# Kernel optimization log

Hardware: AMD Instinct MI355X
Metric: run time of the kernel (lower is better)

The kernel has to match this reference:

```python
import jax, jax.numpy as jnp
import numpy as np

LN_EPS = 1e-12
CHEB_K = 3
HIDDEN = 64


def _layernorm(x, w, b):
    m = jnp.mean(x, axis=-1, keepdims=True)
    v = jnp.mean((x - m) ** 2, axis=-1, keepdims=True)
    return (x - m) / jnp.sqrt(v + LN_EPS) * w + b


def _magcn(x, node_emb, time_emb, ln_w, ln_b, W_pool, b_pool):
    # x: [B,N,C]; node_emb: [N,D]; W_pool: [D,K,C,O]; b_pool: [D,O]
    e = _layernorm(node_emb + time_emb[None, :], ln_w, ln_b)  # dropout = identity (eval)
    supports = jax.nn.softmax(e @ e.T, axis=1)                # [N,N]
    N = e.shape[0]
    Ts = [jnp.eye(N, dtype=x.dtype), supports]
    for _ in range(2, CHEB_K):
        Ts.append(2.0 * supports @ Ts[-1] - Ts[-2])
    S = jnp.stack(Ts, axis=0)                                 # [K,N,N]
    weights = jnp.einsum('nd,dkio->nkio', e, W_pool)          # [N,K,C,O]
    bias = e @ b_pool                                         # [N,O]
    x_g = jnp.einsum('knm,bmc->bnkc', S, x)                   # [B,N,K,C]
    return jnp.einsum('bnki,nkio->bno', x_g, weights) + bias  # [B,N,O]


def setup_inputs() -> dict:
    key = jax.random.key(0)
    ks = jax.random.split(key, 10)
    B, N, C, H, D = 64, 1024, 64, HIDDEN, 16
    return {
        'x': jax.random.normal(ks[0], (B, N, C), jnp.float32),
        'norm_dis_matrix': jax.random.uniform(ks[1], (N, N), jnp.float32),
        'state': jax.random.normal(ks[2], (B, N, H), jnp.float32),
        'node_embeddings': jax.random.normal(ks[3], (N, D), jnp.float32),
        'node_flows': jax.random.normal(ks[4], (B, N), jnp.float32),
        'time_embeddings': jax.random.normal(ks[5], (D,), jnp.float32),
        'gate_W': jax.random.normal(ks[6], (D, CHEB_K, C + H, 2 * H), jnp.float32) * 0.1,
        'gate_b': jax.random.normal(ks[7], (D, 2 * H), jnp.float32) * 0.1,
        'gate_ln_w': jnp.ones((D,), jnp.float32),
        'gate_ln_b': jnp.zeros((D,), jnp.float32),
        'update_W': jax.random.normal(ks[8], (D, CHEB_K, C + H, H), jnp.float32) * 0.1,
        'update_b': jax.random.normal(ks[9], (D, H), jnp.float32) * 0.1,
        'update_ln_w': jnp.ones((D,), jnp.float32),
        'update_ln_b': jnp.zeros((D,), jnp.float32),
    }


def reference(x, norm_dis_matrix, state, node_embeddings, node_flows, time_embeddings,
              gate_W, gate_b, gate_ln_w, gate_ln_b,
              update_W, update_b, update_ln_w, update_ln_b):
    inp_state = jnp.concatenate([x, state], axis=-1)  # [B,N,C+H]
    z_r = jax.nn.sigmoid(_magcn(inp_state, node_embeddings, time_embeddings,
                                gate_ln_w, gate_ln_b, gate_W, gate_b))
    z, r = z_r[..., :HIDDEN], z_r[..., HIDDEN:]
    candidate = jnp.concatenate([x, z * state], axis=-1)
    hc = jnp.tanh(_magcn(candidate, node_embeddings, time_embeddings,
                         update_ln_w, update_ln_b, update_W, update_b))
    return r * state + (1.0 - r) * hc
```

## Files before the change

### kernel.cpp

```cpp
#include <hip/hip_runtime.h>
#include <hip/hip_bf16.h>

typedef __hip_bfloat16 bf16;
typedef __attribute__((ext_vector_type(8))) short bf16x8;
typedef __attribute__((ext_vector_type(4))) float f32x4;

constexpr int Bn = 64;
constexpr int Nn = 1024;
constexpr int Dd = 16;
constexpr int Cc = 64;
constexpr int Hh = 64;
constexpr int CI = 128;
constexpr int OG = 128;
constexpr int OU = 64;
constexpr int Jt = Bn * CI;

__device__ __forceinline__ float b2f(bf16 v) { return __bfloat162float(v); }
__device__ __forceinline__ float lo2f(unsigned u) { return __uint_as_float(u << 16); }
__device__ __forceinline__ float hi2f(unsigned u) { return __uint_as_float(u & 0xffff0000u); }
__device__ __forceinline__ float bfbits2f(unsigned short u) { return __uint_as_float(((unsigned)u) << 16); }
__device__ __forceinline__ unsigned short f2bfbits(float x) {
    bf16 h = __float2bfloat16(x);
    return *reinterpret_cast<unsigned short*>(&h);
}

__device__ __forceinline__ float ldin(const void* p, size_t i, int flag) {
    return flag ? b2f(((const bf16*)p)[i]) : ((const float*)p)[i];
}

__device__ __forceinline__ void gload_lds16(const void* g, void* l) {
    __builtin_amdgcn_global_load_lds((const __attribute__((address_space(1))) void*)g,
                                     (__attribute__((address_space(3))) void*)l, 16, 0, 0);
}

__global__ void detect_kernel(const void* glnw, int* flag) {
    unsigned u = *(const unsigned*)glnw;
    *flag = (u == 0x3F800000u) ? 0 : 1;
}

__global__ void conv_f32(const void* __restrict__ src, float* __restrict__ dst,
                         int n, const int* __restrict__ flag) {
    const int f = *flag;
    for (int i = blockIdx.x * blockDim.x + threadIdx.x; i < n; i += gridDim.x * blockDim.x)
        dst[i] = ldin(src, i, f);
}

__global__ __launch_bounds__(256) void wtrans(const void* __restrict__ src, unsigned short* __restrict__ Wt,
                                              int O, int osh, const int* __restrict__ flag) {
    const int f = *flag;
    const int k0 = blockIdx.x * 64;
    const int d = blockIdx.y;
    __shared__ unsigned short tile[64][136];
    const int t = threadIdx.x;
    for (int idx = t; idx < 64 * O; idx += 256) {
        const int kk = idx >> osh, o = idx & (O - 1);
        tile[kk][o] = f2bfbits(ldin(src, ((size_t)d * 384 + k0 + kk) * O + o, f));
    }
    __syncthreads();
    for (int idx = t; idx < O * 64; idx += 256) {
        const int o = idx >> 6, kk = idx & 63;
        Wt[((size_t)d * O + o) * 384 + k0 + kk] = tile[kk][o];
    }
}

__global__ void ln_kernel(const void* __restrict__ nemb, const void* __restrict__ temb,
                          const void* __restrict__ wg, const void* __restrict__ bg,
                          const void* __restrict__ wu, const void* __restrict__ bu,
                          float* __restrict__ e_g, float* __restrict__ e_u,
                          const int* __restrict__ flag) {
    const int f = *flag;
    int t = blockIdx.x * blockDim.x + threadIdx.x;
    if (t >= 2 * Nn) return;
    int which = t >> 10;
    int n = t & (Nn - 1);
    float v[Dd];
    float mean = 0.f;
#pragma unroll
    for (int d = 0; d < Dd; d++) { v[d] = ldin(nemb, n * Dd + d, f) + ldin(temb, d, f); mean += v[d]; }
    mean *= (1.f / Dd);
    float var = 0.f;
#pragma unroll
    for (int d = 0; d < Dd; d++) { float c = v[d] - mean; var += c * c; }
    var *= (1.f / Dd);
    float inv = 1.f / sqrtf(var + 1e-12f);
    const void* w = which ? wu : wg;
    const void* bb = which ? bu : bg;
    float* e = which ? e_u : e_g;
#pragma unroll
    for (int d = 0; d < Dd; d++)
        e[n * Dd + d] = (v[d] - mean) * inv * ldin(w, d, f) + ldin(bb, d, f);
}

__global__ __launch_bounds__(256) void attn_kernel(const float* __restrict__ e, bf16* __restrict__ A) {
    __shared__ float en[Dd];
    __shared__ float logits[Nn];
    __shared__ float red[256];
    const int n = blockIdx.x, t = threadIdx.x;
    if (t < Dd) en[t] = e[n * Dd + t];
    __syncthreads();
    float lmax = -1e30f;
    for (int m = t; m < Nn; m += 256) {
        float s = 0.f;
#pragma unroll
        for (int d = 0; d < Dd; d++) s += en[d] * e[m * Dd + d];
        logits[m] = s;
        lmax = fmaxf(lmax, s);
    }
    red[t] = lmax; __syncthreads();
    for (int s = 128; s > 0; s >>= 1) { if (t < s) red[t] = fmaxf(red[t], red[t + s]); __syncthreads(); }
    const float M = red[0];
    __syncthreads();
    float lsum = 0.f;
    for (int m = t; m < Nn; m += 256) { float p = expf(logits[m] - M); logits[m] = p; lsum += p; }
    red[t] = lsum; __syncthreads();
    for (int s = 128; s > 0; s >>= 1) { if (t < s) red[t] += red[t + s]; __syncthreads(); }
    const float inv = 1.f / red[0];
    for (int m = t; m < Nn; m += 256) A[(size_t)n * Nn + m] = __float2bfloat16(logits[m] * inv);
}

__global__ __launch_bounds__(256) void build_xg0(const void* __restrict__ x, const void* __restrict__ oth,
                                                 bf16* __restrict__ xg0t, bf16* __restrict__ xg0s,
                                                 const int* __restrict__ flag, int oth_bf16) {
    const int f = *flag;
    const int b = blockIdx.x;
    const int n0 = blockIdx.y * 64;
    __shared__ bf16 tile[128][68];
    const int t = threadIdx.x;
#pragma unroll
    for (int idx = t; idx < 64 * 128; idx += 256) {
        const int n = idx >> 7, i = idx & 127;
        const size_t base = ((size_t)b << 10) + n0 + n;
        float v;
        if (i < Cc) v = ldin(x, base * Cc + i, f);
        else v = oth_bf16 ? b2f(((const bf16*)oth)[base * Hh + i - Cc])
                          : ldin(oth, base * Hh + i - Cc, f);
        tile[i][n] = __float2bfloat16(v);
        xg0s[base * CI + i] = tile[i][n];
    }
    __syncthreads();
#pragma unroll
    for (int idx = t; idx < 128 * 64; idx += 256) {
        const int i = idx >> 6, n = idx & 63;
        xg0t[((size_t)(b * CI + i) << 10) + n0 + n] = tile[i][n];
    }
}

__global__ __launch_bounds__(256) void agg_mfma(const bf16* __restrict__ Amat,
                                                const bf16* __restrict__ Xmat,
                                                const bf16* __restrict__ Sub,
                                                bf16* __restrict__ Ct,
                                                bf16* __restrict__ Cs,
                                                int cheb, int write_t) {
    __shared__ bf16 Atile[128 * 32];
    __shared__ bf16 Xtile[128 * 32];
    char* AtileC = (char*)Atile;
    char* XtileC = (char*)Xtile;

    const int t = threadIdx.x;
    const int lane = t & 63, w = t >> 6;
    const int j0 = blockIdx.x * 128;
    const int m0 = blockIdx.y * 128;
    const int wr = (w >> 1) * 64, wc = (w & 1) * 64;
    const int lr = lane & 15, lq = lane >> 4;

    f32x4 acc[4][4];
#pragma unroll
    for (int a = 0; a < 4; a++)
#pragma unroll
        for (int b = 0; b < 4; b++) acc[a][b] = (f32x4){0.f, 0.f, 0.f, 0.f};

    const int srow = w * 16 + (lane >> 2);
    const int scb = (lane & 3) * 16;

    for (int k0 = 0; k0 < Nn; k0 += 32) {
        __syncthreads();
#pragma unroll
        for (int p = 0; p < 2; p++) {
            const int row = p * 64 + srow;
            gload_lds16((const char*)Amat + (size_t)(m0 + row) * 2048 + k0 * 2 + scb,
                        AtileC + p * 4096 + w * 1024);
            gload_lds16((const char*)Xmat + (size_t)(j0 + row) * 2048 + k0 * 2 + scb,
                        XtileC + p * 4096 + w * 1024);
        }
        __syncthreads();
        bf16x8 af[4], xf[4];
#pragma unroll
        for (int fr = 0; fr < 4; fr++)
            af[fr] = *(const bf16x8*)(AtileC + (wr + fr * 16 + lr) * 64 + lq * 16);
#pragma unroll
        for (int fc = 0; fc < 4; fc++)
            xf[fc] = *(const bf16x8*)(XtileC + (wc + fc * 16 + lr) * 64 + lq * 16);
#pragma unroll
        for (int fr = 0; fr < 4; fr++)
#pragma unroll
            for (int fc = 0; fc < 4; fc++)
                acc[fr][fc] = __builtin_amdgcn_mfma_f32_16x16x32_bf16(af[fr], xf[fc], acc[fr][fc], 0, 0, 0);
    }

#pragma unroll
    for (int fr = 0; fr < 4; fr++) {
        const int m = m0 + wr + fr * 16 + lq * 4;
#pragma unroll
        for (int fc = 0; fc < 4; fc++) {
            const int j = j0 + wc + fc * 16 + lr;
            f32x4 v = acc[fr][fc];
            const size_t off = ((size_t)j << 10) + m;
            if (cheb) {
                const ushort4 s = *(const ushort4*)((const unsigned short*)Sub + off);
                v.x = 2.f * v.x - bfbits2f(s.x);
                v.y = 2.f * v.y - bfbits2f(s.y);
                v.z = 2.f * v.z - bfbits2f(s.z);
                v.w = 2.f * v.w - bfbits2f(s.w);
            }
            ushort4 o4;
            o4.x = f2bfbits(v.x); o4.y = f2bfbits(v.y); o4.z = f2bfbits(v.z); o4.w = f2bfbits(v.w);
            if (write_t) *(ushort4*)((unsigned short*)Ct + off) = o4;
            const int b = j >> 7, i = j & 127;
            unsigned short* ps = (unsigned short*)Cs;
            const unsigned short* pv = (const unsigned short*)&o4;
#pragma unroll
            for (int q = 0; q < 4; q++)
                ps[((((size_t)b << 10) + m + q) << 7) + i] = pv[q];
        }
    }
}

__global__ __launch_bounds__(256, 3) void pernode_gemm(
    const bf16* __restrict__ x0, const bf16* __restrict__ x1, const bf16* __restrict__ x2,
    const float* __restrict__ e, const unsigned short* __restrict__ Wt,
    const float* __restrict__ bpool,
    const void* __restrict__ state, const float* __restrict__ r_in,
    bf16* __restrict__ zs, float* __restrict__ r_out, void* __restrict__ out,
    const int* __restrict__ flag, int OSTR, int gate)
{
    const int f = *flag;
    const int bx = blockIdx.x;
    const int np = gate ? (bx >> 1) : bx;
    const int obase = gate ? ((bx & 1) << 6) : 0;
    const int n0 = np * 2, n1 = n0 + 1;

    __shared__ bf16 Xc[2 * 64 * 128];
    char* XcC = (char*)Xc;

    const int t = threadIdx.x;
    const int lane = t & 63, w = t >> 6;
    const int lr = lane & 15, lq = lane >> 4;
    const int og = obase + w * 16 + lr;

    float en0[16], en1[16];
#pragma unroll
    for (int d = 0; d < 16; d++) { en0[d] = e[n0 * 16 + d]; en1[d] = e[n1 * 16 + d]; }

    f32x4 acc0[4], acc1[4];
#pragma unroll
    for (int i = 0; i < 4; i++) { acc0[i] = (f32x4){0.f,0.f,0.f,0.f}; acc1[i] = (f32x4){0.f,0.f,0.f,0.f}; }

    const bf16* xs[3] = {x0, x1, x2};
    const size_t dstr = (size_t)OSTR * 384;
    const unsigned short* wbase = Wt + (size_t)og * 384;

    for (int ch = 0; ch < 3; ch++) {
        __syncthreads();
        {
            const bf16* Xsrc = xs[ch];
#pragma unroll
            for (int p = 0; p < 8; p++) {
                const int r = w * 32 + p * 4 + (lane >> 4);
                const int nd = r >> 6;
                const int b = r & 63;
                const int g = (lane & 15) ^ (r & 15);
                gload_lds16(Xsrc + (((size_t)b << 10) + (nd ? n1 : n0)) * 128 + g * 8,
                            XcC + (w * 32 + p * 4) * 256);
            }
        }
        for (int ks = 0; ks < 4; ks++) {
            float w0[8], w1[8];
#pragma unroll
            for (int j = 0; j < 8; j++) { w0[j] = 0.f; w1[j] = 0.f; }
            const unsigned short* wp = wbase + ch * 128 + ks * 32 + lq * 8;
#pragma unroll 8
            for (int d = 0; d < 16; d++) {
                const uint4 u = *(const uint4*)(wp + (size_t)d * dstr);
                const float v0 = lo2f(u.x), v1 = hi2f(u.x), v2 = lo2f(u.y), v3 = hi2f(u.y);
                const float v4 = lo2f(u.z), v5 = hi2f(u.z), v6 = lo2f(u.w), v7 = hi2f(u.w);
                const float a = en0[d], b = en1[d];
                w0[0] += a * v0; w0[1] += a * v1; w0[2] += a * v2; w0[3] += a * v3;
                w0[4] += a * v4; w0[5] += a * v5; w0[6] += a * v6; w0[7] += a * v7;
                w1[0] += b * v0; w1[1] += b * v1; w1[2] += b * v2; w1[3] += b * v3;
                w1[4] += b * v4; w1[5] += b * v5; w1[6] += b * v6; w1[7] += b * v7;
            }
            union U8 { bf16x8 v; unsigned short s[8]; } bh0, bl0, bh1, bl1;
#pragma unroll
            for (int j = 0; j < 8; j++) {
                unsigned short h = f2bfbits(w0[j]);
                bh0.s[j] = h; bl0.s[j] = f2bfbits(w0[j] - bfbits2f(h));
                h = f2bfbits(w1[j]);
                bh1.s[j] = h; bl1.s[j] = f2bfbits(w1[j] - bfbits2f(h));
            }
            if (ks == 0) __syncthreads();
#pragma unroll
            for (int mf = 0; mf < 4; mf++) {
                const int row = mf * 16 + lr;
                const int blk = (ks * 4 + lq) ^ lr;
                const bf16x8 af0 = *(const bf16x8*)(XcC + row * 256 + blk * 16);
                const bf16x8 af1 = *(const bf16x8*)(XcC + (64 + row) * 256 + blk * 16);
                acc0[mf] = __builtin_amdgcn_mfma_f32_16x16x32_bf16(af0, bh0.v, acc0[mf], 0, 0, 0);
                acc0[mf] = __builtin_amdgcn_mfma_f32_16x16x32_bf16(af0, bl0.v, acc0[mf], 0, 0, 0);
                acc1[mf] = __builtin_amdgcn_mfma_f32_16x16x32_bf16(af1, bh1.v, acc1[mf], 0, 0, 0);
                acc1[mf] = __builtin_amdgcn_mfma_f32_16x16x32_bf16(af1, bl1.v, acc1[mf], 0, 0, 0);
            }
        }
    }

    float bias0 = 0.f, bias1 = 0.f;
#pragma unroll
    for (int d = 0; d < 16; d++) {
        const float bp = bpool[d * OSTR + og];
        bias0 += en0[d] * bp;
        bias1 += en1[d] * bp;
    }
    const int ol = og & 63;

#pragma unroll
    for (int nd = 0; nd < 2; nd++) {
        const int n_ = nd ? n1 : n0;
        const float bias = nd ? bias1 : bias0;
#pragma unroll
        for (int mf = 0; mf < 4; mf++) {
            const f32x4 a = nd ? acc1[mf] : acc0[mf];
#pragma unroll
            for (int q = 0; q < 4; q++) {
                const int b = mf * 16 + lq * 4 + q;
                const size_t idx = (((size_t)b << 10) + n_) * 64 + ol;
                const float v = a[q] + bias;
                if (gate) {
                    const float sg = 1.f / (1.f + expf(-v));
                    if (obase == 0) {
                        const float st = ldin(state, idx, f);
                        zs[idx] = __float2bfloat16(sg * st);
                    } else {
                        r_out[idx] = sg;
                    }
                } else {
                    const float hc = tanhf(v);
                    const float r = r_in[idx];
                    const float st = ldin(state, idx, f);
                    const float o = r * st + (1.f - r) * hc;
                    if (f) ((bf16*)out)[idx] = __float2bfloat16(o);
                    else   ((float*)out)[idx] = o;
                }
            }
        }
    }
}

extern "C" void kernel_launch(void* const* d_in, const int* in_sizes, int n_in,
                              void* d_out, int out_size, void* d_ws, size_t ws_size,
                              hipStream_t stream) {
    const void* x     = d_in[0];
    const void* state = d_in[2];
    const void* nemb  = d_in[3];
    const void* temb  = d_in[5];
    const void* gW    = d_in[6];
    const void* gb    = d_in[7];
    const void* glnw  = d_in[8];
    const void* glnb  = d_in[9];
    const void* uW    = d_in[10];
    const void* ub    = d_in[11];
    const void* ulnw  = d_in[12];
    const void* ulnb  = d_in[13];

    constexpr int GW_N = Dd * 3 * CI * OG;
    constexpr int GB_N = Dd * OG;
    constexpr int UW_N = Dd * 3 * CI * OU;
    constexpr int UB_N = Dd * OU;

    char* base = (char*)d_ws;
    size_t off = 0;
    auto carve = [&](size_t bytes) { char* p = base + off; off += (bytes + 255) & ~(size_t)255; return p; };
    int*   flag = (int*)carve(4);
    unsigned short* gWt = (unsigned short*)carve(GW_N * 2);
    unsigned short* uWt = (unsigned short*)carve(UW_N * 2);
    float* gbf = (float*)carve(GB_N * 4);
    float* ubf = (float*)carve(UB_N * 4);
    float* e_g = (float*)carve(Nn * Dd * 4);
    float* e_u = (float*)carve(Nn * Dd * 4);
    bf16*  Abf  = (bf16*)carve((size_t)Nn * Nn * 2);
    bf16*  xg0t = (bf16*)carve((size_t)Jt * Nn * 2);
    bf16*  xg0s = (bf16*)carve((size_t)Jt * Nn * 2);
    bf16*  xg1t = (bf16*)carve((size_t)Jt * Nn * 2);
    bf16*  xg1s = (bf16*)carve((size_t)Jt * Nn * 2);
    bf16*  xg2s = (bf16*)carve((size_t)Jt * Nn * 2);
    bf16*  zs   = (bf16*)carve((size_t)Bn * Nn * Hh * 2);
    float* r_s  = (float*)carve((size_t)Bn * Nn * Hh * 4);
    if (ws_size < off) return;

    detect_kernel<<<1, 1, 0, stream>>>(glnw, flag);
    wtrans<<<dim3(6, 16), 256, 0, stream>>>(gW, gWt, OG, 7, flag);
    wtrans<<<dim3(6, 16), 256, 0, stream>>>(uW, uWt, OU, 6, flag);
    conv_f32<<<(GB_N + 255) / 256, 256, 0, stream>>>(gb, gbf, GB_N, flag);
    conv_f32<<<(UB_N + 255) / 256, 256, 0, stream>>>(ub, ubf, UB_N, flag);
    ln_kernel<<<8, 256, 0, stream>>>(nemb, temb, glnw, glnb, ulnw, ulnb, e_g, e_u, flag);

    attn_kernel<<<Nn, 256, 0, stream>>>(e_g, Abf);
    build_xg0<<<dim3(Bn, 16), 256, 0, stream>>>(x, state, xg0t, xg0s, flag, 0);
    agg_mfma<<<dim3(Jt / 128, Nn / 128), 256, 0, stream>>>(Abf, xg0t, nullptr, xg1t, xg1s, 0, 1);
    agg_mfma<<<dim3(Jt / 128, Nn / 128), 256, 0, stream>>>(Abf, xg1t, xg0t, xg1t, xg2s, 1, 0);
    pernode_gemm<<<Nn, 256, 0, stream>>>(xg0s, xg1s, xg2s, e_g, gWt, gbf,
                                         state, nullptr, zs, r_s, nullptr, flag, OG, 1);

    attn_kernel<<<Nn, 256, 0, stream>>>(e_u, Abf);
    build_xg0<<<dim3(Bn, 16), 256, 0, stream>>>(x, zs, xg0t, xg0s, flag, 1);
    agg_mfma<<<dim3(Jt / 128, Nn / 128), 256, 0, stream>>>(Abf, xg0t, nullptr, xg1t, xg1s, 0, 1);
    agg_mfma<<<dim3(Jt / 128, Nn / 128), 256, 0, stream>>>(Abf, xg1t, xg0t, xg1t, xg2s, 1, 0);
    pernode_gemm<<<Nn / 2, 256, 0, stream>>>(xg0s, xg1s, xg2s, e_u, uWt, ubf,
                                             state, r_s, nullptr, nullptr, d_out, flag, OU, 0);
}
```

Baseline: 570.3 us.

## Stage agg output transpose through LDS and tile per-node GEMM weights in LDS

agg_mfma now writes its node-major output through a padded LDS tile and emits coalesced 16-byte stores, replacing the scattered 2-byte strided stores. pernode_gemm is templated on nodes per block (4 for the gate pass, 2 for the update pass). Each block stages weight slices and X tiles into LDS with global_load_lds, so the pooled weights are reused across more nodes, and the node embeddings are made wave-uniform with readfirstlane. In exchange, the extra LDS use and the launch-bounds drop to 2 blocks per SM may lower occupancy, and more syncs are added per k-step.

```diff
diff --git a/kernel.cpp b/kernel.cpp
--- a/kernel.cpp
+++ b/kernel.cpp
@@ -22,6 +22,9 @@
 __device__ __forceinline__ unsigned short f2bfbits(float x) {
     bf16 h = __float2bfloat16(x);
     return *reinterpret_cast<unsigned short*>(&h);
+}
+__device__ __forceinline__ float rfl(float x) {
+    return __int_as_float(__builtin_amdgcn_readfirstlane(__float_as_int(x)));
 }
 
 __device__ __forceinline__ float ldin(const void* p, size_t i, int flag) {
@@ -153,6 +156,7 @@
                                                 int cheb, int write_t) {
     __shared__ bf16 Atile[128 * 32];
     __shared__ bf16 Xtile[128 * 32];
+    __shared__ unsigned short Ts[128 * 136];
     char* AtileC = (char*)Atile;
     char* XtileC = (char*)Xtile;
 
@@ -199,10 +203,12 @@
 
 #pragma unroll
     for (int fr = 0; fr < 4; fr++) {
-        const int m = m0 + wr + fr * 16 + lq * 4;
+        const int ml = wr + fr * 16 + lq * 4;
+        const int m = m0 + ml;
 #pragma unroll
         for (int fc = 0; fc < 4; fc++) {
-            const int j = j0 + wc + fc * 16 + lr;
+            const int i = wc + fc * 16 + lr;
+            const int j = j0 + i;
             f32x4 v = acc[fr][fc];
             const size_t off = ((size_t)j << 10) + m;
             if (cheb) {
@@ -215,125 +221,148 @@
             ushort4 o4;
             o4.x = f2bfbits(v.x); o4.y = f2bfbits(v.y); o4.z = f2bfbits(v.z); o4.w = f2bfbits(v.w);
             if (write_t) *(ushort4*)((unsigned short*)Ct + off) = o4;
-            const int b = j >> 7, i = j & 127;
-            unsigned short* ps = (unsigned short*)Cs;
             const unsigned short* pv = (const unsigned short*)&o4;
 #pragma unroll
-            for (int q = 0; q < 4; q++)
-                ps[((((size_t)b << 10) + m + q) << 7) + i] = pv[q];
+            for (int q = 0; q < 4; q++) Ts[(ml + q) * 136 + i] = pv[q];
         }
     }
-}
-
-__global__ __launch_bounds__(256, 3) void pernode_gemm(
+    __syncthreads();
+    const int b = j0 >> 7;
+#pragma unroll
+    for (int p = 0; p < 8; p++) {
+        const int u = p * 256 + t;
+        const int m = u >> 4, ig = (u & 15) * 8;
+        const uint4 val = *(const uint4*)&Ts[m * 136 + ig];
+        *(uint4*)((unsigned short*)Cs + (((size_t)b << 10) + m0 + m) * 128 + ig) = val;
+    }
+}
+
+template<int G, int GATE>
+__global__ __launch_bounds__(256, 2) void pernode_gemm(
     const bf16* __restrict__ x0, const bf16* __restrict__ x1, const bf16* __restrict__ x2,
     const float* __restrict__ e, const unsigned short* __restrict__ Wt,
     const float* __restrict__ bpool,
     const void* __restrict__ state, const float* __restrict__ r_in,
     bf16* __restrict__ zs, float* __restrict__ r_out, void* __restrict__ out,
-    const int* __restrict__ flag, int OSTR, int gate)
+    const int* __restrict__ flag)
 {
+    constexpr int OSTR = GATE ? 128 : 64;
     const int f = *flag;
     const int bx = blockIdx.x;
-    const int np = gate ? (bx >> 1) : bx;
-    const int obase = gate ? ((bx & 1) << 6) : 0;
-    const int n0 = np * 2, n1 = n0 + 1;
-
-    __shared__ bf16 Xc[2 * 64 * 128];
-    char* XcC = (char*)Xc;
+    const int grp = GATE ? (bx >> 1) : bx;
+    const int obase = GATE ? ((bx & 1) << 6) : 0;
+    const int n0 = grp * G;
+
+    __shared__ bf16 Wl[8 * 64 * 32];
+    __shared__ bf16 Xl[G * 64 * 32];
+    char* WlC = (char*)Wl;
+    char* XlC = (char*)Xl;
 
     const int t = threadIdx.x;
     const int lane = t & 63, w = t >> 6;
     const int lr = lane & 15, lq = lane >> 4;
     const int og = obase + w * 16 + lr;
 
-    float en0[16], en1[16];
-#pragma unroll
-    for (int d = 0; d < 16; d++) { en0[d] = e[n0 * 16 + d]; en1[d] = e[n1 * 16 + d]; }
-
-    f32x4 acc0[4], acc1[4];
-#pragma unroll
-    for (int i = 0; i < 4; i++) { acc0[i] = (f32x4){0.f,0.f,0.f,0.f}; acc1[i] = (f32x4){0.f,0.f,0.f,0.f}; }
+    float en[G][16];
+#pragma unroll
+    for (int nl = 0; nl < G; nl++)
+#pragma unroll
+        for (int d = 0; d < 16; d++) en[nl][d] = rfl(e[(n0 + nl) * 16 + d]);
+
+    f32x4 acc[G][4];
+#pragma unroll
+    for (int nl = 0; nl < G; nl++)
+#pragma unroll
+        for (int mt = 0; mt < 4; mt++) acc[nl][mt] = (f32x4){0.f, 0.f, 0.f, 0.f};
 
     const bf16* xs[3] = {x0, x1, x2};
-    const size_t dstr = (size_t)OSTR * 384;
-    const unsigned short* wbase = Wt + (size_t)og * 384;
-
+
+#pragma unroll 1
     for (int ch = 0; ch < 3; ch++) {
-        __syncthreads();
-        {
-            const bf16* Xsrc = xs[ch];
-#pragma unroll
-            for (int p = 0; p < 8; p++) {
-                const int r = w * 32 + p * 4 + (lane >> 4);
-                const int nd = r >> 6;
-                const int b = r & 63;
-                const int g = (lane & 15) ^ (r & 15);
-                gload_lds16(Xsrc + (((size_t)b << 10) + (nd ? n1 : n0)) * 128 + g * 8,
-                            XcC + (w * 32 + p * 4) * 256);
+        const bf16* Xsrc = xs[ch];
+#pragma unroll 1
+        for (int ks = 0; ks < 4; ks++) {
+            float wacc[G][8];
+#pragma unroll
+            for (int nl = 0; nl < G; nl++)
+#pragma unroll
+                for (int j = 0; j < 8; j++) wacc[nl][j] = 0.f;
+
+#pragma unroll
+            for (int dh = 0; dh < 2; dh++) {
+                __syncthreads();
+#pragma unroll
+                for (int p = 0; p < 8; p++) {
+                    const int u = p * 256 + w * 64 + lane;
+                    const int r = u >> 2, kg = u & 3;
+                    const int d = r >> 6, ol = r & 63;
+                    gload_lds16(Wt + ((size_t)((dh * 8 + d) * OSTR + obase + ol) * 384)
+                                   + ch * 128 + ks * 32 + kg * 8,
+                                WlC + u * 16);
+                }
+                if (dh == 0) {
+#pragma unroll
+                    for (int p = 0; p < G; p++) {
+                        const int u = p * 256 + w * 64 + lane;
+                        const int r = u >> 2, kg = u & 3;
+                        const int nl = r >> 6, b = r & 63;
+                        gload_lds16(Xsrc + (((size_t)b << 10) + n0 + nl) * 128 + ks * 32 + kg * 8,
+                                    XlC + u * 16);
+                    }
+                }
+                __syncthreads();
+#pragma unroll
+                for (int d = 0; d < 8; d++) {
+                    const bf16x8 wv = *(const bf16x8*)(WlC + (d * 64 + w * 16 + lr) * 64 + lq * 16);
+                    const unsigned* wu = (const unsigned*)&wv;
+                    float v[8];
+                    v[0] = lo2f(wu[0]); v[1] = hi2f(wu[0]);
+                    v[2] = lo2f(wu[1]); v[3] = hi2f(wu[1]);
+                    v[4] = lo2f(wu[2]); v[5] = hi2f(wu[2]);
+                    v[6] = lo2f(wu[3]); v[7] = hi2f(wu[3]);
+#pragma unroll
+                    for (int nl = 0; nl < G; nl++) {
+                        const float ed = en[nl][dh * 8 + d];
+#pragma unroll
+                        for (int j = 0; j < 8; j++) wacc[nl][j] += ed * v[j];
+                    }
+                }
+            }
+#pragma unroll
+            for (int nl = 0; nl < G; nl++) {
+                union U8 { bf16x8 v; unsigned short s[8]; } bh, bl;
+#pragma unroll
+                for (int j = 0; j < 8; j++) {
+                    const unsigned short h = f2bfbits(wacc[nl][j]);
+                    bh.s[j] = h;
+                    bl.s[j] = f2bfbits(wacc[nl][j] - bfbits2f(h));
+                }
+#pragma unroll
+                for (int mt = 0; mt < 4; mt++) {
+                    const bf16x8 af = *(const bf16x8*)(XlC + (nl * 64 + mt * 16 + lr) * 64 + lq * 16);
+                    acc[nl][mt] = __builtin_amdgcn_mfma_f32_16x16x32_bf16(af, bh.v, acc[nl][mt], 0, 0, 0);
+                    acc[nl][mt] = __builtin_amdgcn_mfma_f32_16x16x32_bf16(af, bl.v, acc[nl][mt], 0, 0, 0);
+                }
             }
         }
-        for (int ks = 0; ks < 4; ks++) {
-            float w0[8], w1[8];
-#pragma unroll
-            for (int j = 0; j < 8; j++) { w0[j] = 0.f; w1[j] = 0.f; }
-            const unsigned short* wp = wbase + ch * 128 + ks * 32 + lq * 8;
-#pragma unroll 8
-            for (int d = 0; d < 16; d++) {
-                const uint4 u = *(const uint4*)(wp + (size_t)d * dstr);
-                const float v0 = lo2f(u.x), v1 = hi2f(u.x), v2 = lo2f(u.y), v3 = hi2f(u.y);
-                const float v4 = lo2f(u.z), v5 = hi2f(u.z), v6 = lo2f(u.w), v7 = hi2f(u.w);
-                const float a = en0[d], b = en1[d];
-                w0[0] += a * v0; w0[1] += a * v1; w0[2] += a * v2; w0[3] += a * v3;
-                w0[4] += a * v4; w0[5] += a * v5; w0[6] += a * v6; w0[7] += a * v7;
-                w1[0] += b * v0; w1[1] += b * v1; w1[2] += b * v2; w1[3] += b * v3;
-                w1[4] += b * v4; w1[5] += b * v5; w1[6] += b * v6; w1[7] += b * v7;
-            }
-            union U8 { bf16x8 v; unsigned short s[8]; } bh0, bl0, bh1, bl1;
-#pragma unroll
-            for (int j = 0; j < 8; j++) {
-                unsigned short h = f2bfbits(w0[j]);
-                bh0.s[j] = h; bl0.s[j] = f2bfbits(w0[j] - bfbits2f(h));
-                h = f2bfbits(w1[j]);
-                bh1.s[j] = h; bl1.s[j] = f2bfbits(w1[j] - bfbits2f(h));
-            }
-            if (ks == 0) __syncthreads();
-#pragma unroll
-            for (int mf = 0; mf < 4; mf++) {
-                const int row = mf * 16 + lr;
-                const int blk = (ks * 4 + lq) ^ lr;
-                const bf16x8 af0 = *(const bf16x8*)(XcC + row * 256 + blk * 16);
-                const bf16x8 af1 = *(const bf16x8*)(XcC + (64 + row) * 256 + blk * 16);
-                acc0[mf] = __builtin_amdgcn_mfma_f32_16x16x32_bf16(af0, bh0.v, acc0[mf], 0, 0, 0);
-                acc0[mf] = __builtin_amdgcn_mfma_f32_16x16x32_bf16(af0, bl0.v, acc0[mf], 0, 0, 0);
-                acc1[mf] = __builtin_amdgcn_mfma_f32_16x16x32_bf16(af1, bh1.v, acc1[mf], 0, 0, 0);
-                acc1[mf] = __builtin_amdgcn_mfma_f32_16x16x32_bf16(af1, bl1.v, acc1[mf], 0, 0, 0);
-            }
-        }
-    }
-
-    float bias0 = 0.f, bias1 = 0.f;
-#pragma unroll
-    for (int d = 0; d < 16; d++) {
-        const float bp = bpool[d * OSTR + og];
-        bias0 += en0[d] * bp;
-        bias1 += en1[d] * bp;
-    }
+    }
+
     const int ol = og & 63;
-
-#pragma unroll
-    for (int nd = 0; nd < 2; nd++) {
-        const int n_ = nd ? n1 : n0;
-        const float bias = nd ? bias1 : bias0;
-#pragma unroll
-        for (int mf = 0; mf < 4; mf++) {
-            const f32x4 a = nd ? acc1[mf] : acc0[mf];
+#pragma unroll
+    for (int nl = 0; nl < G; nl++) {
+        const int n_ = n0 + nl;
+        float bias = 0.f;
+#pragma unroll
+        for (int d = 0; d < 16; d++) bias += en[nl][d] * bpool[d * OSTR + og];
+#pragma unroll
+        for (int mt = 0; mt < 4; mt++) {
+            const f32x4 a = acc[nl][mt];
 #pragma unroll
             for (int q = 0; q < 4; q++) {
-                const int b = mf * 16 + lq * 4 + q;
+                const int b = mt * 16 + lq * 4 + q;
                 const size_t idx = (((size_t)b << 10) + n_) * 64 + ol;
                 const float v = a[q] + bias;
-                if (gate) {
+                if (GATE) {
                     const float sg = 1.f / (1.f + expf(-v));
                     if (obase == 0) {
                         const float st = ldin(state, idx, f);
@@ -406,13 +435,13 @@
     build_xg0<<<dim3(Bn, 16), 256, 0, stream>>>(x, state, xg0t, xg0s, flag, 0);
     agg_mfma<<<dim3(Jt / 128, Nn / 128), 256, 0, stream>>>(Abf, xg0t, nullptr, xg1t, xg1s, 0, 1);
     agg_mfma<<<dim3(Jt / 128, Nn / 128), 256, 0, stream>>>(Abf, xg1t, xg0t, xg1t, xg2s, 1, 0);
-    pernode_gemm<<<Nn, 256, 0, stream>>>(xg0s, xg1s, xg2s, e_g, gWt, gbf,
-                                         state, nullptr, zs, r_s, nullptr, flag, OG, 1);
+    pernode_gemm<4, 1><<<512, 256, 0, stream>>>(xg0s, xg1s, xg2s, e_g, gWt, gbf,
+                                                state, nullptr, zs, r_s, nullptr, flag);
 
     attn_kernel<<<Nn, 256, 0, stream>>>(e_u, Abf);
     build_xg0<<<dim3(Bn, 16), 256, 0, stream>>>(x, zs, xg0t, xg0s, flag, 1);
     agg_mfma<<<dim3(Jt / 128, Nn / 128), 256, 0, stream>>>(Abf, xg0t, nullptr, xg1t, xg1s, 0, 1);
     agg_mfma<<<dim3(Jt / 128, Nn / 128), 256, 0, stream>>>(Abf, xg1t, xg0t, xg1t, xg2s, 1, 0);
-    pernode_gemm<<<Nn / 2, 256, 0, stream>>>(xg0s, xg1s, xg2s, e_u, uWt, ubf,
-                                             state, r_s, nullptr, nullptr, d_out, flag, OU, 0);
-}
+    pernode_gemm<2, 0><<<512, 256, 0, stream>>>(xg0s, xg1s, xg2s, e_u, uWt, ubf,
+                                                state, r_s, nullptr, nullptr, d_out, flag);
+}
```

Result: faster. 473.6 us (-17.0%).
